# Performance work log

Hardware: AMD Instinct MI355X
Metric: run time of the kernel (lower is better)

Reference implementation:

```python
import jax, jax.numpy as jnp
import numpy as np

B, C, CB, WIDTH = 16, 256, 64, 32
F = CB * WIDTH  # lstm_features = 2048


def setup_inputs() -> dict:
    key = jax.random.key(0)
    ks = jax.random.split(key, 14)
    s = 0.02  # ~1/sqrt(F), torch default uniform(-1/sqrt(h), 1/sqrt(h)) scale
    return {
        "x": jax.random.normal(ks[0], (B, C, WIDTH, WIDTH), jnp.float32),
        "w_in": jax.random.normal(ks[1], (CB, C), jnp.float32) * s,
        "b_in": jax.random.normal(ks[2], (CB,), jnp.float32) * s,
        "W_ih0": jax.random.normal(ks[3], (4 * F, F), jnp.float32) * s,
        "W_hh0": jax.random.normal(ks[4], (4 * F, F), jnp.float32) * s,
        "b_ih0": jax.random.normal(ks[5], (4 * F,), jnp.float32) * s,
        "b_hh0": jax.random.normal(ks[6], (4 * F,), jnp.float32) * s,
        "W_ih1": jax.random.normal(ks[7], (4 * F, F), jnp.float32) * s,
        "W_hh1": jax.random.normal(ks[8], (4 * F, F), jnp.float32) * s,
        "b_ih1": jax.random.normal(ks[9], (4 * F,), jnp.float32) * s,
        "b_hh1": jax.random.normal(ks[10], (4 * F,), jnp.float32) * s,
        "w_out": jax.random.normal(ks[11], (C, CB), jnp.float32) * s,
        "b_out": jax.random.normal(ks[12], (C,), jnp.float32) * s,
    }


def _lstm_cell(x_t, h, c, W_ih, W_hh, b_ih, b_hh):
    # torch nn.LSTM gate order: i, f, g, o
    g = x_t @ W_ih.T + h @ W_hh.T + (b_ih + b_hh)
    i, f, gg, o = jnp.split(g, 4, axis=-1)
    c_n = jax.nn.sigmoid(f) * c + jax.nn.sigmoid(i) * jnp.tanh(gg)
    h_n = jax.nn.sigmoid(o) * jnp.tanh(c_n)
    return h_n, c_n


def reference(x, w_in, b_in, W_ih0, W_hh0, b_ih0, b_hh0,
              W_ih1, W_hh1, b_ih1, b_hh1, w_out, b_out):
    Bn, Cn, H, W = x.shape
    # 1x1 conv bottleneck in -> [B, Cb, H, W]
    bn = jnp.einsum('bchw,oc->bohw', x, w_in) + b_in[None, :, None, None]
    Cb = bn.shape[1]
    Ff = W * Cb
    # rows as sequence: [H, B, W*Cb], feature index = w*Cb + c
    seq = bn.transpose(2, 0, 3, 1).reshape(H, Bn, Ff)

    def step(states, x_t):
        h0, c0, h1, c1 = states
        h0, c0 = _lstm_cell(x_t, h0, c0, W_ih0, W_hh0, b_ih0, b_hh0)
        h1, c1 = _lstm_cell(h0, h1, c1, W_ih1, W_hh1, b_ih1, b_hh1)
        return (h0, c0, h1, c1), h1

    z = jnp.zeros((Bn, Ff), x.dtype)
    states, outs = jax.lax.scan(step, (z, z, z, z), seq)
    y0 = outs[-1]  # out[-1]: first generated row

    def gen(carry, _):
        st, y = carry
        st, y_n = step(st, y)
        return (st, y_n), y_n

    _, gen_outs = jax.lax.scan(gen, (states, y0), None, length=W - 1)
    seq_out = jnp.concatenate([y0[None], gen_outs], axis=0)  # [W, B, F]

    # un-flatten back to spatial: [B, S=W, W, Cb] then 1x1 conv out -> [B, C, S, W]
    spatial = seq_out.transpose(1, 0, 2).reshape(Bn, W, W, Cb)
    y = jnp.einsum('bswc,oc->bosw', spatial, w_out) + b_out[None, :, None, None]
    # stitch generated rows below input along height dim
    return jnp.concatenate([x, y], axis=2)
```

## Files before the change

kernel.cpp:

```cpp
#include <hip/hip_runtime.h>
#include <hip/hip_bf16.h>

typedef unsigned short u16;
typedef unsigned char uchar;
typedef unsigned long long u64;
typedef float f32x4 __attribute__((ext_vector_type(4)));
typedef int i8v __attribute__((ext_vector_type(8)));

#define FDIM 2048
#define NBLK 256
#define NCELL 126

__device__ __forceinline__ u16 f2b(float x) {
    __hip_bfloat16 h = __float2bfloat16(x);
    return __builtin_bit_cast(u16, h);
}
__device__ __forceinline__ float b2f(u16 u) {
    __hip_bfloat16 h = __builtin_bit_cast(__hip_bfloat16, u);
    return __bfloat162float(h);
}
__device__ __forceinline__ float sigm(float x) { return 1.0f / (1.0f + __expf(-x)); }
__device__ __forceinline__ float tanh_f(float x) { return 1.0f - 2.0f / (__expf(2.0f * x) + 1.0f); }

__device__ __forceinline__ unsigned f2fp8(float x) {
    unsigned u = __builtin_bit_cast(unsigned, x);
    unsigned s = (u >> 24) & 0x80u;
    unsigned mag = u & 0x7fffffffu;
    if (mag >= 0x43E80000u) return s | 0x7Eu;
    int e = (int)(mag >> 23) - 127;
    if (e >= -6) {
        unsigned m = mag + 0x7FFFFu + ((mag >> 20) & 1u);
        unsigned e8 = (m >> 23) - 127 + 7;
        unsigned m3 = (m >> 20) & 7u;
        if (e8 >= 16u) return s | 0x7Eu;
        return s | (e8 << 3) | m3;
    }
    float ax = __builtin_bit_cast(float, mag);
    int d = (int)__builtin_rintf(ax * 512.0f);
    return s | (unsigned)d;
}

__device__ __forceinline__ unsigned q_e2m1(float v) {
    unsigned s = (v < 0.f) ? 8u : 0u;
    float a = fabsf(v);
    unsigned q;
    if (a < 0.25f) q = 0;
    else if (a < 0.75f) q = 1;
    else if (a < 1.25f) q = 2;
    else if (a < 1.75f) q = 3;
    else if (a < 2.5f)  q = 4;
    else if (a < 3.5f)  q = 5;
    else if (a < 5.0f)  q = 6;
    else q = 7;
    return s | q;
}

__global__ __launch_bounds__(256) void k_pack4(const float* __restrict__ W0, const float* __restrict__ W1,
                                               const float* __restrict__ W2, const float* __restrict__ W3,
                                               uchar* __restrict__ Wp4, uchar* __restrict__ scl) {
    __shared__ float lw[32][132];
    int idx = blockIdx.x;
    int kt = idx & 15, mat = (idx >> 4) & 3, bl = idx >> 6;
    const float* src = mat == 0 ? W0 : mat == 1 ? W1 : mat == 2 ? W2 : W3;
    int tid = threadIdx.x;
    for (int i = tid; i < 32 * 32; i += 256) {
        int r = i >> 5, c4 = i & 31;
        const float* p = src + (size_t)((r >> 3) * 2048 + bl * 8 + (r & 7)) * 2048 + kt * 128 + c4 * 4;
        float4 v = *(const float4*)p;
        lw[r][c4 * 4 + 0] = v.x; lw[r][c4 * 4 + 1] = v.y;
        lw[r][c4 * 4 + 2] = v.z; lw[r][c4 * 4 + 3] = v.w;
    }
    __syncthreads();
    if (tid < 128) {
        int gp = tid >> 6, lane = tid & 63;
        int r = (2 * gp + ((lane & 15) >> 3)) * 8 + (lane & 7);
        int k0 = (lane >> 4) * 32;
        float mx = 0.f;
#pragma unroll
        for (int e = 0; e < 32; ++e) mx = fmaxf(mx, fabsf(lw[r][k0 + e]));
        int ee = -127;
        if (mx > 0.f) {
            ee = (int)ceilf(log2f(mx * (1.0f / 6.0f)));
            if (ee < -127) ee = -127;
            if (ee > 127) ee = 127;
        }
        float inv = exp2f((float)(-ee));
        unsigned wd[4];
#pragma unroll
        for (int d = 0; d < 4; ++d) {
            unsigned acc = 0;
#pragma unroll
            for (int bi = 0; bi < 4; ++bi) {
                float v0 = lw[r][k0 + d * 8 + 2 * bi] * inv;
                float v1 = lw[r][k0 + d * 8 + 2 * bi + 1] * inv;
                acc |= (q_e2m1(v0) << (bi * 8)) | (q_e2m1(v1) << (bi * 8 + 4));
            }
            wd[d] = acc;
        }
        size_t wo = (size_t)bl * 131072 + (((size_t)(mat * 2 + gp) * 16 + (size_t)kt) * 64 + lane) * 16;
        *(uint4*)(Wp4 + wo) = make_uint4(wd[0], wd[1], wd[2], wd[3]);
        scl[(((size_t)bl * 4 + mat) * 2 + gp) * 1024 + (size_t)lane * 16 + kt] = (uchar)(ee + 127);
    }
}

__global__ void k_bias(const float* __restrict__ bi0, const float* __restrict__ bh0,
                       const float* __restrict__ bi1, const float* __restrict__ bh1,
                       float* __restrict__ bias0, float* __restrict__ bias1) {
    int i = blockIdx.x * blockDim.x + threadIdx.x;
    if (i < 4 * FDIM) {
        bias0[i] = bi0[i] + bh0[i];
        bias1[i] = bi1[i] + bh1[i];
    }
}

__global__ __launch_bounds__(256) void k_seqprep(const float* __restrict__ x,
                                                 const float* __restrict__ w_in,
                                                 const float* __restrict__ b_in,
                                                 uchar* __restrict__ seqb) {
    int h = blockIdx.x >> 4, b = blockIdx.x & 15;
    __shared__ float xs[256][32];
    __shared__ float wl[64][257];
    int tid = threadIdx.x;
    for (int i = tid; i < 256 * 32; i += 256) {
        int c = i >> 5, w = i & 31;
        xs[c][w] = x[(((size_t)b * 256 + c) * 32 + h) * 32 + w];
    }
    for (int i = tid; i < 64 * 256; i += 256) {
        int cb = i >> 8, c = i & 255;
        wl[cb][c] = w_in[i];
    }
    __syncthreads();
    int w = (tid * 8) >> 6, cb0 = (tid * 8) & 63;
    float acc[8];
#pragma unroll
    for (int j = 0; j < 8; ++j) acc[j] = b_in[cb0 + j];
    for (int c = 0; c < 256; ++c) {
        float xv = xs[c][w];
#pragma unroll
        for (int j = 0; j < 8; ++j) acc[j] += xv * wl[cb0 + j][c];
    }
    unsigned lo = 0, hi2 = 0;
#pragma unroll
    for (int j = 0; j < 4; ++j) lo |= f2fp8(acc[j] * 4.0f) << (j * 8);
#pragma unroll
    for (int j = 0; j < 4; ++j) hi2 |= f2fp8(acc[4 + j] * 4.0f) << (j * 8);
    int kt = tid >> 4, kq = (tid >> 2) & 3, e0 = (tid & 3) * 8;
    uchar* dst = seqb + (size_t)h * 32768 + (size_t)kt * 2048 + (size_t)(b + 16 * kq) * 32 + e0;
    *(uint2*)dst = make_uint2(lo, hi2);
}

__global__ __launch_bounds__(512, 1) void k_lstm(const uchar* __restrict__ Wp4,
                                                 const uchar* __restrict__ scl,
                                                 const float* __restrict__ bias0,
                                                 const float* __restrict__ bias1,
                                                 const uchar* __restrict__ seqb,
                                                 uchar* __restrict__ H0, uchar* __restrict__ H1,
                                                 u16* __restrict__ seqout,
                                                 unsigned* __restrict__ cnts) {
    __shared__ uchar wlds[131072];
    __shared__ float gbuf[2][8][16][20];
    __shared__ u64 hs_st[16];
    __shared__ unsigned flagLDS;
    const int tid = threadIdx.x, lane = tid & 63, w = tid >> 6;
    const int gp = w & 1, m = (w >> 1) & 1, kh = w >> 2;
    const int bl = blockIdx.x;
    const size_t BF = (size_t)16 * FDIM;

    {
        const uchar* src = Wp4 + (size_t)bl * 131072;
        for (int i = tid; i < 8192; i += 512)
            *(uint4*)(wlds + (size_t)i * 16) = *(const uint4*)(src + (size_t)i * 16);
    }
    uint4 scl0 = *(const uint4*)(scl + (((size_t)bl * 4 + m) * 2 + gp) * 1024 + (size_t)lane * 16);
    uint4 scl1 = *(const uint4*)(scl + (((size_t)bl * 4 + 2 + m) * 2 + gp) * 1024 + (size_t)lane * 16);

    float bw0[2][4], bw1[2][4];
    float cs0[2] = {0.f, 0.f}, cs1[2] = {0.f, 0.f};
    if (w == 7) {
        const int f0 = (lane & 3) * 2;
#pragma unroll
        for (int i = 0; i < 2; ++i) {
            int col = bl * 8 + f0 + i;
#pragma unroll
            for (int g = 0; g < 4; ++g) {
                bw0[i][g] = bias0[g * FDIM + col];
                bw1[i][g] = bias1[g * FDIM + col];
            }
        }
    }
    if (tid == 0) flagLDS = 0;
    __syncthreads();

    const int b16 = lane & 15, kq = lane >> 4;
    for (int c = 0; c < NCELL; ++c) {
        const int s = c >> 1, isL1 = c & 1, par = c & 1;
        const uchar* xsrc = isL1 ? (H0 + (size_t)(s + 1) * BF)
                          : (s < 32 ? (seqb + (size_t)s * BF) : (H1 + (size_t)s * BF));
        const uchar* hsrc = isL1 ? (H1 + (size_t)s * BF) : (H0 + (size_t)s * BF);
        const uchar* asrc = m ? hsrc : xsrc;
        const int tgt = m ? (c - 1) : ((isL1 || s >= 32) ? c : 0);
        if (w == 0) {
            if (tgt > 0) {
                const unsigned need = 4u * (unsigned)tgt;
                while (__hip_atomic_load(cnts + (size_t)lane * 32,
                                         __ATOMIC_RELAXED, __HIP_MEMORY_SCOPE_AGENT) < need)
                    __builtin_amdgcn_s_sleep(2);
                if (lane == 0)
                    __hip_atomic_store(&flagLDS, (unsigned)tgt,
                                       __ATOMIC_RELAXED, __HIP_MEMORY_SCOPE_WORKGROUP);
            }
        } else if (tgt > 0) {
            while (__hip_atomic_load(&flagLDS, __ATOMIC_RELAXED,
                                     __HIP_MEMORY_SCOPE_WORKGROUP) < (unsigned)tgt)
                __builtin_amdgcn_s_sleep(1);
        }
        asm volatile("" ::: "memory");

        const uchar* ap = asrc + (size_t)lane * 32;
        const uchar* bp = wlds + (size_t)((isL1 * 2 + m) * 2 + gp) * 16384 + lane * 16;
        uint4 sv = isL1 ? scl1 : scl0;
        unsigned sw0 = kh ? sv.z : sv.x;
        unsigned sw1 = kh ? sv.w : sv.y;

        uint4 A[8][2];
#pragma unroll
        for (int t = 0; t < 8; ++t) {
            A[t][0] = *(const uint4*)(ap + (size_t)(kh * 8 + t) * 2048);
            A[t][1] = *(const uint4*)(ap + (size_t)(kh * 8 + t) * 2048 + 16);
        }
        f32x4 acc0 = {0.f, 0.f, 0.f, 0.f}, acc1 = {0.f, 0.f, 0.f, 0.f};
#define MF(T, SW, J)                                                                   \
        {                                                                              \
            uint4 alo = A[T][0], ahi = A[T][1];                                        \
            uint4 bb = *(const uint4*)(bp + (kh * 8 + (T)) * 1024);                    \
            i8v av = {(int)alo.x, (int)alo.y, (int)alo.z, (int)alo.w,                  \
                      (int)ahi.x, (int)ahi.y, (int)ahi.z, (int)ahi.w};                 \
            i8v bv = {(int)bb.x, (int)bb.y, (int)bb.z, (int)bb.w, 0, 0, 0, 0};         \
            if ((T) & 1)                                                               \
                acc1 = __builtin_amdgcn_mfma_scale_f32_16x16x128_f8f6f4(               \
                    av, bv, acc1, 0, 4, 0, 127, J, (int)(SW));                         \
            else                                                                       \
                acc0 = __builtin_amdgcn_mfma_scale_f32_16x16x128_f8f6f4(               \
                    av, bv, acc0, 0, 4, 0, 127, J, (int)(SW));                         \
        }
        MF(0, sw0, 0); MF(1, sw0, 1); MF(2, sw0, 2); MF(3, sw0, 3);
        MF(4, sw1, 0); MF(5, sw1, 1); MF(6, sw1, 2); MF(7, sw1, 3);
#undef MF
        f32x4 acc = acc0 + acc1;
#pragma unroll
        for (int i = 0; i < 4; ++i) gbuf[par][w][kq * 4 + i][b16] = acc[i];
        __syncthreads();

        if (w == 7) {
            const int b = lane >> 2, f0 = (lane & 3) * 2;
            u16 hb2 = 0;
            float hnv[2];
#pragma unroll
            for (int i = 0; i < 2; ++i) {
                const int f = f0 + i;
                float gv[4];
#pragma unroll
                for (int g = 0; g < 4; ++g) {
                    int gpp = g >> 1, jl = ((g & 1) << 3) | f;
                    gv[g] = (gbuf[par][gpp][b][jl] + gbuf[par][gpp + 2][b][jl]
                           + gbuf[par][gpp + 4][b][jl] + gbuf[par][gpp + 6][b][jl]) * 0.25f
                           + (isL1 ? bw1[i][g] : bw0[i][g]);
                }
                float co = isL1 ? cs1[i] : cs0[i];
                float cn = sigm(gv[1]) * co + sigm(gv[0]) * tanh_f(gv[2]);
                float hn = sigm(gv[3]) * tanh_f(cn);
                if (isL1) cs1[i] = cn; else cs0[i] = cn;
                hb2 |= (u16)(f2fp8(hn * 4.0f) << (8 * i));
                hnv[i] = hn;
            }
            *(u16*)((uchar*)&hs_st[b] + f0) = hb2;
            asm volatile("s_waitcnt lgkmcnt(0)" ::: "memory");
            if (lane < 16) {
                uchar* hdst = (isL1 ? H1 : H0) + (size_t)(s + 1) * BF;
                size_t o = (size_t)(bl >> 4) * 2048 + (size_t)((bl >> 2) & 3) * 512
                         + (size_t)(bl & 3) * 8 + (size_t)lane * 32;
                __hip_atomic_store((u64*)(hdst + o), hs_st[lane],
                                   __ATOMIC_RELAXED, __HIP_MEMORY_SCOPE_AGENT);
            }
            asm volatile("s_waitcnt vmcnt(0)" ::: "memory");
            if (lane == 0)
                __hip_atomic_fetch_add(cnts + (size_t)(bl & 63) * 32, 1u,
                                       __ATOMIC_RELAXED, __HIP_MEMORY_SCOPE_AGENT);
            if (isL1 && s >= 31) {
                unsigned pk = (unsigned)f2b(hnv[0]) | ((unsigned)f2b(hnv[1]) << 16);
                *(unsigned*)(seqout + (size_t)(s - 31) * BF + (size_t)b * FDIM + bl * 8 + f0) = pk;
            }
        }
    }
}

__global__ void k_copyx(const float* __restrict__ x, float* __restrict__ out) {
    size_t n = (size_t)4096 * 256;
    size_t stride = (size_t)gridDim.x * blockDim.x;
    for (size_t i = (size_t)blockIdx.x * blockDim.x + threadIdx.x; i < n; i += stride) {
        size_t bc = i >> 8, r = i & 255;
        ((float4*)out)[bc * 512 + r] = ((const float4*)x)[i];
    }
}

__global__ __launch_bounds__(256) void k_convout(const u16* __restrict__ seqout,
                                                 const float* __restrict__ w_out,
                                                 const float* __restrict__ b_out,
                                                 float* __restrict__ out) {
    int s = blockIdx.x >> 4, b = blockIdx.x & 15;
    __shared__ float srow[2048];
    int tid = threadIdx.x;
    for (int i = tid; i < 2048; i += 256) srow[i] = b2f(seqout[((size_t)s * 16 + b) * FDIM + i]);
    __syncthreads();
    int o = tid;
    float bo = b_out[o];
    float wreg[64];
#pragma unroll
    for (int cb = 0; cb < 64; ++cb) wreg[cb] = w_out[o * 64 + cb];
    for (int w4 = 0; w4 < 8; ++w4) {
        float ac0 = bo, ac1 = bo, ac2 = bo, ac3 = bo;
#pragma unroll
        for (int cb = 0; cb < 64; ++cb) {
            float wv = wreg[cb];
            ac0 += srow[(w4 * 4 + 0) * 64 + cb] * wv;
            ac1 += srow[(w4 * 4 + 1) * 64 + cb] * wv;
            ac2 += srow[(w4 * 4 + 2) * 64 + cb] * wv;
            ac3 += srow[(w4 * 4 + 3) * 64 + cb] * wv;
        }
        float4 v; v.x = ac0; v.y = ac1; v.z = ac2; v.w = ac3;
        *(float4*)&out[(((size_t)b * 256 + o) * 64 + 32 + s) * 32 + w4 * 4] = v;
    }
}

extern "C" void kernel_launch(void* const* d_in, const int* in_sizes, int n_in,
                              void* d_out, int out_size, void* d_ws, size_t ws_size,
                              hipStream_t stream) {
    const float* x    = (const float*)d_in[0];
    const float* w_in = (const float*)d_in[1];
    const float* b_in = (const float*)d_in[2];
    const float* Wih0 = (const float*)d_in[3];
    const float* Whh0 = (const float*)d_in[4];
    const float* bih0 = (const float*)d_in[5];
    const float* bhh0 = (const float*)d_in[6];
    const float* Wih1 = (const float*)d_in[7];
    const float* Whh1 = (const float*)d_in[8];
    const float* bih1 = (const float*)d_in[9];
    const float* bhh1 = (const float*)d_in[10];
    const float* wout = (const float*)d_in[11];
    const float* bout = (const float*)d_in[12];
    float* out = (float*)d_out;
    char* ws = (char*)d_ws;
    const size_t BF = (size_t)16 * FDIM;

    uchar* Wp4 = (uchar*)ws;
    size_t off = (size_t)NBLK * 131072;
    uchar* scl = (uchar*)(ws + off); off += (size_t)NBLK * 4 * 2 * 1024;
    float* bias0 = (float*)(ws + off); off += 4 * FDIM * 4;
    float* bias1 = (float*)(ws + off); off += 4 * FDIM * 4;
    uchar* seqb = (uchar*)(ws + off); off += (size_t)32 * BF;
    u16* seqout = (u16*)(ws + off); off += (size_t)32 * BF * 2;
    uchar* H0 = (uchar*)(ws + off); off += (size_t)64 * BF;
    uchar* H1 = (uchar*)(ws + off); off += (size_t)64 * BF;
    off = (off + 127) & ~(size_t)127;
    unsigned* cnts = (unsigned*)(ws + off); size_t cntoff = off; off += 64 * 32 * 4;

    hipMemsetAsync(H0, 0, BF, stream);
    hipMemsetAsync(H1, 0, BF, stream);
    hipMemsetAsync(ws + cntoff, 0, off - cntoff, stream);

    k_pack4<<<256 * 4 * 16, 256, 0, stream>>>(Wih0, Whh0, Wih1, Whh1, Wp4, scl);
    k_bias<<<32, 256, 0, stream>>>(bih0, bhh0, bih1, bhh1, bias0, bias1);
    k_seqprep<<<512, 256, 0, stream>>>(x, w_in, b_in, seqb);
    k_lstm<<<NBLK, 512, 0, stream>>>(Wp4, scl, bias0, bias1, seqb, H0, H1, seqout, cnts);
    k_copyx<<<2048, 256, 0, stream>>>(x, out);
    k_convout<<<512, 256, 0, stream>>>(seqout, wout, bout, out);
}
```

Baseline: 629.2 us.

## Replace counter barrier with per-cell block tags and repartition warps by K quarters

Each block now writes a per-cell, per-block tag instead of bumping shared atomic counters. Warp 0 polls all 256 tags for the previous cell, and for the static-input cells it polls only after its own MFMA work so that fetching and compute overlap the wait. The warp split changes from gate-pair by K-half to K-quarter, with each warp covering both gate groups. Partial sums are combined through LDS atomicAdd into a zeroed buffer rather than an 8-way strided reduction. This aims to cut contention on the counters and the length of the reduction, at the cost of LDS atomics, wider polling and a larger tag array to memset.

```diff
diff --git a/kernel.cpp b/kernel.cpp
--- a/kernel.cpp
+++ b/kernel.cpp
@@ -156,13 +156,13 @@
                                                  const uchar* __restrict__ seqb,
                                                  uchar* __restrict__ H0, uchar* __restrict__ H1,
                                                  u16* __restrict__ seqout,
-                                                 unsigned* __restrict__ cnts) {
+                                                 unsigned* __restrict__ tags) {
     __shared__ uchar wlds[131072];
-    __shared__ float gbuf[2][8][16][20];
+    __shared__ float gbuf[2][2][16][20];
     __shared__ u64 hs_st[16];
     __shared__ unsigned flagLDS;
     const int tid = threadIdx.x, lane = tid & 63, w = tid >> 6;
-    const int gp = w & 1, m = (w >> 1) & 1, kh = w >> 2;
+    const int m = w >> 2, q = w & 3;
     const int bl = blockIdx.x;
     const size_t BF = (size_t)16 * FDIM;
 
@@ -171,8 +171,13 @@
         for (int i = tid; i < 8192; i += 512)
             *(uint4*)(wlds + (size_t)i * 16) = *(const uint4*)(src + (size_t)i * 16);
     }
-    uint4 scl0 = *(const uint4*)(scl + (((size_t)bl * 4 + m) * 2 + gp) * 1024 + (size_t)lane * 16);
-    uint4 scl1 = *(const uint4*)(scl + (((size_t)bl * 4 + 2 + m) * 2 + gp) * 1024 + (size_t)lane * 16);
+    unsigned scw[4][2];
+#pragma unroll
+    for (int mt = 0; mt < 4; ++mt)
+#pragma unroll
+        for (int g = 0; g < 2; ++g)
+            scw[mt][g] = *(const unsigned*)(scl + (((size_t)bl * 4 + mt) * 2 + g) * 1024
+                                            + (size_t)lane * 16 + q * 4);
 
     float bw0[2][4], bw1[2][4];
     float cs0[2] = {0.f, 0.f}, cs1[2] = {0.f, 0.f};
@@ -188,6 +193,7 @@
             }
         }
     }
+    for (int i = tid; i < 2 * 2 * 16 * 20; i += 512) ((float*)gbuf)[i] = 0.f;
     if (tid == 0) flagLDS = 0;
     __syncthreads();
 
@@ -198,57 +204,80 @@
                           : (s < 32 ? (seqb + (size_t)s * BF) : (H1 + (size_t)s * BF));
         const uchar* hsrc = isL1 ? (H1 + (size_t)s * BF) : (H0 + (size_t)s * BF);
         const uchar* asrc = m ? hsrc : xsrc;
-        const int tgt = m ? (c - 1) : ((isL1 || s >= 32) ? c : 0);
-        if (w == 0) {
-            if (tgt > 0) {
-                const unsigned need = 4u * (unsigned)tgt;
-                while (__hip_atomic_load(cnts + (size_t)lane * 32,
-                                         __ATOMIC_RELAXED, __HIP_MEMORY_SCOPE_AGENT) < need)
-                    __builtin_amdgcn_s_sleep(2);
-                if (lane == 0)
-                    __hip_atomic_store(&flagLDS, (unsigned)tgt,
-                                       __ATOMIC_RELAXED, __HIP_MEMORY_SCOPE_WORKGROUP);
-            }
-        } else if (tgt > 0) {
-            while (__hip_atomic_load(&flagLDS, __ATOMIC_RELAXED,
-                                     __HIP_MEMORY_SCOPE_WORKGROUP) < (unsigned)tgt)
+        const bool staticX = (!isL1 && s < 32);
+
+        const bool pollBefore = (w == 0) && (c >= 1) && !staticX;
+        const bool pollAfter  = (w == 0) && (c >= 1) && staticX;
+        if (pollBefore) {
+            const unsigned* trow = tags + (size_t)(c - 1) * 256 + lane * 4;
+            for (;;) {
+                unsigned v0 = __hip_atomic_load(trow + 0, __ATOMIC_RELAXED, __HIP_MEMORY_SCOPE_AGENT);
+                unsigned v1 = __hip_atomic_load(trow + 1, __ATOMIC_RELAXED, __HIP_MEMORY_SCOPE_AGENT);
+                unsigned v2 = __hip_atomic_load(trow + 2, __ATOMIC_RELAXED, __HIP_MEMORY_SCOPE_AGENT);
+                unsigned v3 = __hip_atomic_load(trow + 3, __ATOMIC_RELAXED, __HIP_MEMORY_SCOPE_AGENT);
+                if ((v0 & v1 & v2 & v3) == 1u) break;
                 __builtin_amdgcn_s_sleep(1);
+            }
+            if (lane == 0)
+                __hip_atomic_store(&flagLDS, (unsigned)c, __ATOMIC_RELAXED, __HIP_MEMORY_SCOPE_WORKGROUP);
+        } else if (w != 0) {
+            unsigned need = m ? ((c >= 2) ? (unsigned)(c - 1) : 0u)
+                             : (staticX ? 0u : (unsigned)c);
+            if (need)
+                while (__hip_atomic_load(&flagLDS, __ATOMIC_RELAXED,
+                                         __HIP_MEMORY_SCOPE_WORKGROUP) < need)
+                    __builtin_amdgcn_s_sleep(1);
         }
         asm volatile("" ::: "memory");
 
         const uchar* ap = asrc + (size_t)lane * 32;
-        const uchar* bp = wlds + (size_t)((isL1 * 2 + m) * 2 + gp) * 16384 + lane * 16;
-        uint4 sv = isL1 ? scl1 : scl0;
-        unsigned sw0 = kh ? sv.z : sv.x;
-        unsigned sw1 = kh ? sv.w : sv.y;
-
-        uint4 A[8][2];
-#pragma unroll
-        for (int t = 0; t < 8; ++t) {
-            A[t][0] = *(const uint4*)(ap + (size_t)(kh * 8 + t) * 2048);
-            A[t][1] = *(const uint4*)(ap + (size_t)(kh * 8 + t) * 2048 + 16);
-        }
-        f32x4 acc0 = {0.f, 0.f, 0.f, 0.f}, acc1 = {0.f, 0.f, 0.f, 0.f};
-#define MF(T, SW, J)                                                                   \
+        uint4 A[4][2];
+#pragma unroll
+        for (int t = 0; t < 4; ++t) {
+            A[t][0] = *(const uint4*)(ap + (size_t)(q * 4 + t) * 2048);
+            A[t][1] = *(const uint4*)(ap + (size_t)(q * 4 + t) * 2048 + 16);
+        }
+        const int mat = isL1 * 2 + m;
+        const uchar* bp0 = wlds + (size_t)(mat * 2 + 0) * 16384 + lane * 16;
+        const uchar* bp1 = wlds + (size_t)(mat * 2 + 1) * 16384 + lane * 16;
+        const unsigned s0w = scw[mat][0], s1w = scw[mat][1];
+
+        f32x4 a00 = {0.f,0.f,0.f,0.f}, a01 = {0.f,0.f,0.f,0.f};
+        f32x4 a10 = {0.f,0.f,0.f,0.f}, a11 = {0.f,0.f,0.f,0.f};
+#define MF(T, G)                                                                       \
         {                                                                              \
             uint4 alo = A[T][0], ahi = A[T][1];                                        \
-            uint4 bb = *(const uint4*)(bp + (kh * 8 + (T)) * 1024);                    \
+            uint4 bb = *(const uint4*)(((G) ? bp1 : bp0) + (q * 4 + (T)) * 1024);      \
             i8v av = {(int)alo.x, (int)alo.y, (int)alo.z, (int)alo.w,                  \
                       (int)ahi.x, (int)ahi.y, (int)ahi.z, (int)ahi.w};                 \
             i8v bv = {(int)bb.x, (int)bb.y, (int)bb.z, (int)bb.w, 0, 0, 0, 0};         \
-            if ((T) & 1)                                                               \
-                acc1 = __builtin_amdgcn_mfma_scale_f32_16x16x128_f8f6f4(               \
-                    av, bv, acc1, 0, 4, 0, 127, J, (int)(SW));                         \
-            else                                                                       \
-                acc0 = __builtin_amdgcn_mfma_scale_f32_16x16x128_f8f6f4(               \
-                    av, bv, acc0, 0, 4, 0, 127, J, (int)(SW));                         \
-        }
-        MF(0, sw0, 0); MF(1, sw0, 1); MF(2, sw0, 2); MF(3, sw0, 3);
-        MF(4, sw1, 0); MF(5, sw1, 1); MF(6, sw1, 2); MF(7, sw1, 3);
+            f32x4& ac = (G) ? (((T) & 1) ? a11 : a10) : (((T) & 1) ? a01 : a00);       \
+            ac = __builtin_amdgcn_mfma_scale_f32_16x16x128_f8f6f4(                     \
+                av, bv, ac, 0, 4, 0, 127, T, (int)((G) ? s1w : s0w));                  \
+        }
+        MF(0, 0) MF(1, 0) MF(2, 0) MF(3, 0)
+        MF(0, 1) MF(1, 1) MF(2, 1) MF(3, 1)
 #undef MF
-        f32x4 acc = acc0 + acc1;
-#pragma unroll
-        for (int i = 0; i < 4; ++i) gbuf[par][w][kq * 4 + i][b16] = acc[i];
+        f32x4 accJ0 = a00 + a01, accJ1 = a10 + a11;
+#pragma unroll
+        for (int i = 0; i < 4; ++i) {
+            atomicAdd(&gbuf[par][0][kq * 4 + i][b16], accJ0[i]);
+            atomicAdd(&gbuf[par][1][kq * 4 + i][b16], accJ1[i]);
+        }
+
+        if (pollAfter) {
+            const unsigned* trow = tags + (size_t)(c - 1) * 256 + lane * 4;
+            for (;;) {
+                unsigned v0 = __hip_atomic_load(trow + 0, __ATOMIC_RELAXED, __HIP_MEMORY_SCOPE_AGENT);
+                unsigned v1 = __hip_atomic_load(trow + 1, __ATOMIC_RELAXED, __HIP_MEMORY_SCOPE_AGENT);
+                unsigned v2 = __hip_atomic_load(trow + 2, __ATOMIC_RELAXED, __HIP_MEMORY_SCOPE_AGENT);
+                unsigned v3 = __hip_atomic_load(trow + 3, __ATOMIC_RELAXED, __HIP_MEMORY_SCOPE_AGENT);
+                if ((v0 & v1 & v2 & v3) == 1u) break;
+                __builtin_amdgcn_s_sleep(1);
+            }
+            if (lane == 0)
+                __hip_atomic_store(&flagLDS, (unsigned)c, __ATOMIC_RELAXED, __HIP_MEMORY_SCOPE_WORKGROUP);
+        }
         __syncthreads();
 
         if (w == 7) {
@@ -262,9 +291,7 @@
 #pragma unroll
                 for (int g = 0; g < 4; ++g) {
                     int gpp = g >> 1, jl = ((g & 1) << 3) | f;
-                    gv[g] = (gbuf[par][gpp][b][jl] + gbuf[par][gpp + 2][b][jl]
-                           + gbuf[par][gpp + 4][b][jl] + gbuf[par][gpp + 6][b][jl]) * 0.25f
-                           + (isL1 ? bw1[i][g] : bw0[i][g]);
+                    gv[g] = gbuf[par][gpp][b][jl] * 0.25f + (isL1 ? bw1[i][g] : bw0[i][g]);
                 }
                 float co = isL1 ? cs1[i] : cs0[i];
                 float cn = sigm(gv[1]) * co + sigm(gv[0]) * tanh_f(gv[2]);
@@ -273,6 +300,14 @@
                 hb2 |= (u16)(f2fp8(hn * 4.0f) << (8 * i));
                 hnv[i] = hn;
             }
+#pragma unroll
+            for (int i = 0; i < 2; ++i) {
+                const int f = f0 + i;
+#pragma unroll
+                for (int g = 0; g < 4; ++g)
+                    gbuf[par][g >> 1][b][((g & 1) << 3) | f] = 0.f;
+            }
+            *(u16*)((uchar*)&hs_st[b]) ;
             *(u16*)((uchar*)&hs_st[b] + f0) = hb2;
             asm volatile("s_waitcnt lgkmcnt(0)" ::: "memory");
             if (lane < 16) {
@@ -284,8 +319,8 @@
             }
             asm volatile("s_waitcnt vmcnt(0)" ::: "memory");
             if (lane == 0)
-                __hip_atomic_fetch_add(cnts + (size_t)(bl & 63) * 32, 1u,
-                                       __ATOMIC_RELAXED, __HIP_MEMORY_SCOPE_AGENT);
+                __hip_atomic_store(tags + (size_t)c * 256 + bl, 1u,
+                                   __ATOMIC_RELAXED, __HIP_MEMORY_SCOPE_AGENT);
             if (isL1 && s >= 31) {
                 unsigned pk = (unsigned)f2b(hnv[0]) | ((unsigned)f2b(hnv[1]) << 16);
                 *(unsigned*)(seqout + (size_t)(s - 31) * BF + (size_t)b * FDIM + bl * 8 + f0) = pk;
@@ -362,16 +397,17 @@
     uchar* H0 = (uchar*)(ws + off); off += (size_t)64 * BF;
     uchar* H1 = (uchar*)(ws + off); off += (size_t)64 * BF;
     off = (off + 127) & ~(size_t)127;
-    unsigned* cnts = (unsigned*)(ws + off); size_t cntoff = off; off += 64 * 32 * 4;
+    unsigned* tags = (unsigned*)(ws + off); size_t tagoff = off;
+    off += (size_t)NCELL * 256 * 4;
 
     hipMemsetAsync(H0, 0, BF, stream);
     hipMemsetAsync(H1, 0, BF, stream);
-    hipMemsetAsync(ws + cntoff, 0, off - cntoff, stream);
+    hipMemsetAsync(ws + tagoff, 0, off - tagoff, stream);
 
     k_pack4<<<256 * 4 * 16, 256, 0, stream>>>(Wih0, Whh0, Wih1, Whh1, Wp4, scl);
     k_bias<<<32, 256, 0, stream>>>(bih0, bhh0, bih1, bhh1, bias0, bias1);
     k_seqprep<<<512, 256, 0, stream>>>(x, w_in, b_in, seqb);
-    k_lstm<<<NBLK, 512, 0, stream>>>(Wp4, scl, bias0, bias1, seqb, H0, H1, seqout, cnts);
+    k_lstm<<<NBLK, 512, 0, stream>>>(Wp4, scl, bias0, bias1, seqb, H0, H1, seqout, tags);
     k_copyx<<<2048, 256, 0, stream>>>(x, out);
     k_convout<<<512, 256, 0, stream>>>(seqout, wout, bout, out);
 }
```

New measurement: 1.266 ms. 101% more time.

## Replace shared counters with per-cell tag flags polled by a dedicated wave

Applied to the files above, without the earlier changes.

The grid-wide dependency tracking changes from 64 atomically incremented counters to one tag word per block per cell, each written with a plain store. A ninth wave now does the global polling and publishes progress to the other waves through an LDS flag, so the compute waves only spin on LDS. A-operand loads are also rotated by block index to spread memory traffic. In exchange the block is larger, and the tag array plus its memset grows to one row per cell.

```diff
diff --git a/kernel.cpp b/kernel.cpp
--- a/kernel.cpp
+++ b/kernel.cpp
@@ -149,14 +149,14 @@
     *(uint2*)dst = make_uint2(lo, hi2);
 }
 
-__global__ __launch_bounds__(512, 1) void k_lstm(const uchar* __restrict__ Wp4,
+__global__ __launch_bounds__(576, 1) void k_lstm(const uchar* __restrict__ Wp4,
                                                  const uchar* __restrict__ scl,
                                                  const float* __restrict__ bias0,
                                                  const float* __restrict__ bias1,
                                                  const uchar* __restrict__ seqb,
                                                  uchar* __restrict__ H0, uchar* __restrict__ H1,
                                                  u16* __restrict__ seqout,
-                                                 unsigned* __restrict__ cnts) {
+                                                 unsigned* __restrict__ tags) {
     __shared__ uchar wlds[131072];
     __shared__ float gbuf[2][8][16][20];
     __shared__ u64 hs_st[16];
@@ -168,11 +168,14 @@
 
     {
         const uchar* src = Wp4 + (size_t)bl * 131072;
-        for (int i = tid; i < 8192; i += 512)
+        for (int i = tid; i < 8192; i += 576)
             *(uint4*)(wlds + (size_t)i * 16) = *(const uint4*)(src + (size_t)i * 16);
     }
-    uint4 scl0 = *(const uint4*)(scl + (((size_t)bl * 4 + m) * 2 + gp) * 1024 + (size_t)lane * 16);
-    uint4 scl1 = *(const uint4*)(scl + (((size_t)bl * 4 + 2 + m) * 2 + gp) * 1024 + (size_t)lane * 16);
+    uint4 scl0, scl1;
+    if (w < 8) {
+        scl0 = *(const uint4*)(scl + (((size_t)bl * 4 + m) * 2 + gp) * 1024 + (size_t)lane * 16);
+        scl1 = *(const uint4*)(scl + (((size_t)bl * 4 + 2 + m) * 2 + gp) * 1024 + (size_t)lane * 16);
+    }
 
     float bw0[2][4], bw1[2][4];
     float cs0[2] = {0.f, 0.f}, cs1[2] = {0.f, 0.f};
@@ -197,58 +200,72 @@
         const uchar* xsrc = isL1 ? (H0 + (size_t)(s + 1) * BF)
                           : (s < 32 ? (seqb + (size_t)s * BF) : (H1 + (size_t)s * BF));
         const uchar* hsrc = isL1 ? (H1 + (size_t)s * BF) : (H0 + (size_t)s * BF);
-        const uchar* asrc = m ? hsrc : xsrc;
-        const int tgt = m ? (c - 1) : ((isL1 || s >= 32) ? c : 0);
-        if (w == 0) {
-            if (tgt > 0) {
-                const unsigned need = 4u * (unsigned)tgt;
-                while (__hip_atomic_load(cnts + (size_t)lane * 32,
-                                         __ATOMIC_RELAXED, __HIP_MEMORY_SCOPE_AGENT) < need)
-                    __builtin_amdgcn_s_sleep(2);
+        const bool staticX = (!isL1 && s < 32);
+
+        if (w == 8) {
+            if (c >= 1) {
+                const unsigned* trow = tags + (size_t)(c - 1) * 2048;
+                for (;;) {
+                    unsigned v0 = __hip_atomic_load(trow + (size_t)lane * 8,
+                                                    __ATOMIC_RELAXED, __HIP_MEMORY_SCOPE_AGENT);
+                    unsigned v1 = __hip_atomic_load(trow + (size_t)(lane + 64) * 8,
+                                                    __ATOMIC_RELAXED, __HIP_MEMORY_SCOPE_AGENT);
+                    unsigned v2 = __hip_atomic_load(trow + (size_t)(lane + 128) * 8,
+                                                    __ATOMIC_RELAXED, __HIP_MEMORY_SCOPE_AGENT);
+                    unsigned v3 = __hip_atomic_load(trow + (size_t)(lane + 192) * 8,
+                                                    __ATOMIC_RELAXED, __HIP_MEMORY_SCOPE_AGENT);
+                    if ((v0 & v1 & v2 & v3) == 1u) break;
+                    __builtin_amdgcn_s_sleep(1);
+                }
                 if (lane == 0)
-                    __hip_atomic_store(&flagLDS, (unsigned)tgt,
+                    __hip_atomic_store(&flagLDS, (unsigned)c,
                                        __ATOMIC_RELAXED, __HIP_MEMORY_SCOPE_WORKGROUP);
             }
-        } else if (tgt > 0) {
-            while (__hip_atomic_load(&flagLDS, __ATOMIC_RELAXED,
-                                     __HIP_MEMORY_SCOPE_WORKGROUP) < (unsigned)tgt)
-                __builtin_amdgcn_s_sleep(1);
-        }
-        asm volatile("" ::: "memory");
-
-        const uchar* ap = asrc + (size_t)lane * 32;
-        const uchar* bp = wlds + (size_t)((isL1 * 2 + m) * 2 + gp) * 16384 + lane * 16;
-        uint4 sv = isL1 ? scl1 : scl0;
-        unsigned sw0 = kh ? sv.z : sv.x;
-        unsigned sw1 = kh ? sv.w : sv.y;
-
-        uint4 A[8][2];
-#pragma unroll
-        for (int t = 0; t < 8; ++t) {
-            A[t][0] = *(const uint4*)(ap + (size_t)(kh * 8 + t) * 2048);
-            A[t][1] = *(const uint4*)(ap + (size_t)(kh * 8 + t) * 2048 + 16);
-        }
-        f32x4 acc0 = {0.f, 0.f, 0.f, 0.f}, acc1 = {0.f, 0.f, 0.f, 0.f};
+        } else {
+            const uchar* asrc = m ? hsrc : xsrc;
+            unsigned need = m ? ((c >= 2) ? (unsigned)(c - 1) : 0u)
+                             : (staticX ? 0u : (unsigned)c);
+            if (need)
+                while (__hip_atomic_load(&flagLDS, __ATOMIC_RELAXED,
+                                         __HIP_MEMORY_SCOPE_WORKGROUP) < need)
+                    __builtin_amdgcn_s_sleep(1);
+            asm volatile("" ::: "memory");
+
+            const uchar* ap = asrc + (size_t)lane * 32;
+            uint4 A[8][2];
+#pragma unroll
+            for (int t = 0; t < 8; ++t) {
+                int tt = (t + bl) & 7;
+                A[tt][0] = *(const uint4*)(ap + (size_t)(kh * 8 + tt) * 2048);
+                A[tt][1] = *(const uint4*)(ap + (size_t)(kh * 8 + tt) * 2048 + 16);
+            }
+            const uchar* bp = wlds + (size_t)((isL1 * 2 + m) * 2 + gp) * 16384 + lane * 16;
+            uint4 sv = isL1 ? scl1 : scl0;
+            unsigned sw0 = kh ? sv.z : sv.x;
+            unsigned sw1 = kh ? sv.w : sv.y;
+
+            f32x4 acc0 = {0.f, 0.f, 0.f, 0.f}, acc1 = {0.f, 0.f, 0.f, 0.f};
 #define MF(T, SW, J)                                                                   \
-        {                                                                              \
-            uint4 alo = A[T][0], ahi = A[T][1];                                        \
-            uint4 bb = *(const uint4*)(bp + (kh * 8 + (T)) * 1024);                    \
-            i8v av = {(int)alo.x, (int)alo.y, (int)alo.z, (int)alo.w,                  \
-                      (int)ahi.x, (int)ahi.y, (int)ahi.z, (int)ahi.w};                 \
-            i8v bv = {(int)bb.x, (int)bb.y, (int)bb.z, (int)bb.w, 0, 0, 0, 0};         \
-            if ((T) & 1)                                                               \
-                acc1 = __builtin_amdgcn_mfma_scale_f32_16x16x128_f8f6f4(               \
-                    av, bv, acc1, 0, 4, 0, 127, J, (int)(SW));                         \
-            else                                                                       \
-                acc0 = __builtin_amdgcn_mfma_scale_f32_16x16x128_f8f6f4(               \
-                    av, bv, acc0, 0, 4, 0, 127, J, (int)(SW));                         \
-        }
-        MF(0, sw0, 0); MF(1, sw0, 1); MF(2, sw0, 2); MF(3, sw0, 3);
-        MF(4, sw1, 0); MF(5, sw1, 1); MF(6, sw1, 2); MF(7, sw1, 3);
+            {                                                                          \
+                uint4 alo = A[T][0], ahi = A[T][1];                                    \
+                uint4 bb = *(const uint4*)(bp + (kh * 8 + (T)) * 1024);                \
+                i8v av = {(int)alo.x, (int)alo.y, (int)alo.z, (int)alo.w,              \
+                          (int)ahi.x, (int)ahi.y, (int)ahi.z, (int)ahi.w};             \
+                i8v bv = {(int)bb.x, (int)bb.y, (int)bb.z, (int)bb.w, 0, 0, 0, 0};     \
+                if ((T) & 1)                                                           \
+                    acc1 = __builtin_amdgcn_mfma_scale_f32_16x16x128_f8f6f4(           \
+                        av, bv, acc1, 0, 4, 0, 127, J, (int)(SW));                     \
+                else                                                                   \
+                    acc0 = __builtin_amdgcn_mfma_scale_f32_16x16x128_f8f6f4(           \
+                        av, bv, acc0, 0, 4, 0, 127, J, (int)(SW));                     \
+            }
+            MF(0, sw0, 0); MF(1, sw0, 1); MF(2, sw0, 2); MF(3, sw0, 3);
+            MF(4, sw1, 0); MF(5, sw1, 1); MF(6, sw1, 2); MF(7, sw1, 3);
 #undef MF
-        f32x4 acc = acc0 + acc1;
-#pragma unroll
-        for (int i = 0; i < 4; ++i) gbuf[par][w][kq * 4 + i][b16] = acc[i];
+            f32x4 acc = acc0 + acc1;
+#pragma unroll
+            for (int i = 0; i < 4; ++i) gbuf[par][w][kq * 4 + i][b16] = acc[i];
+        }
         __syncthreads();
 
         if (w == 7) {
@@ -284,8 +301,8 @@
             }
             asm volatile("s_waitcnt vmcnt(0)" ::: "memory");
             if (lane == 0)
-                __hip_atomic_fetch_add(cnts + (size_t)(bl & 63) * 32, 1u,
-                                       __ATOMIC_RELAXED, __HIP_MEMORY_SCOPE_AGENT);
+                __hip_atomic_store(tags + (size_t)c * 2048 + (size_t)bl * 8, 1u,
+                                   __ATOMIC_RELAXED, __HIP_MEMORY_SCOPE_AGENT);
             if (isL1 && s >= 31) {
                 unsigned pk = (unsigned)f2b(hnv[0]) | ((unsigned)f2b(hnv[1]) << 16);
                 *(unsigned*)(seqout + (size_t)(s - 31) * BF + (size_t)b * FDIM + bl * 8 + f0) = pk;
@@ -362,16 +379,17 @@
     uchar* H0 = (uchar*)(ws + off); off += (size_t)64 * BF;
     uchar* H1 = (uchar*)(ws + off); off += (size_t)64 * BF;
     off = (off + 127) & ~(size_t)127;
-    unsigned* cnts = (unsigned*)(ws + off); size_t cntoff = off; off += 64 * 32 * 4;
+    unsigned* tags = (unsigned*)(ws + off); size_t tagoff = off;
+    off += (size_t)NCELL * 2048 * 4;
 
     hipMemsetAsync(H0, 0, BF, stream);
     hipMemsetAsync(H1, 0, BF, stream);
-    hipMemsetAsync(ws + cntoff, 0, off - cntoff, stream);
+    hipMemsetAsync(ws + tagoff, 0, off - tagoff, stream);
 
     k_pack4<<<256 * 4 * 16, 256, 0, stream>>>(Wih0, Whh0, Wih1, Whh1, Wp4, scl);
     k_bias<<<32, 256, 0, stream>>>(bih0, bhh0, bih1, bhh1, bias0, bias1);
     k_seqprep<<<512, 256, 0, stream>>>(x, w_in, b_in, seqb);
-    k_lstm<<<NBLK, 512, 0, stream>>>(Wp4, scl, bias0, bias1, seqb, H0, H1, seqout, cnts);
+    k_lstm<<<NBLK, 576, 0, stream>>>(Wp4, scl, bias0, bias1, seqb, H0, H1, seqout, tags);
     k_copyx<<<2048, 256, 0, stream>>>(x, out);
     k_convout<<<512, 256, 0, stream>>>(seqout, wout, bout, out);
 }
```

After: 1.558 ms. 2.48x slower.
